# Optimization experiments

Hardware: AMD Instinct MI355X
Metric: run time of the kernel (lower is better)

The kernel has to match this reference:

```python
import jax, jax.numpy as jnp
import numpy as np

NUM_CAPSULE = 10
DIM_CAPSULE = 16
ROUTINGS = 3
EPS = 1e-7  # K.epsilon()


def squash(x, axis=-1):
    # bojone squash: x / sqrt(s2 + eps) * s2 / (1 + s2)
    s2 = jnp.sum(jnp.square(x), axis=axis, keepdims=True)
    return x * s2 / ((1.0 + s2) * jnp.sqrt(s2 + EPS))


def setup_inputs() -> dict:
    key = jax.random.key(0)
    k1, k2 = jax.random.split(key)
    B, N, D_in = 64, 2048, 128  # batch, input_num_capsule, input_dim_capsule
    u_vecs = jax.random.normal(k1, (B, N, D_in), dtype=jnp.float32)
    fan_out = NUM_CAPSULE * DIM_CAPSULE
    limit = float(np.sqrt(6.0 / (D_in + fan_out)))  # glorot_uniform
    W = jax.random.uniform(k2, (D_in, fan_out), dtype=jnp.float32,
                           minval=-limit, maxval=limit)
    return {"u_vecs": u_vecs, "W": W}


def reference(u_vecs, W):
    B, N, _ = u_vecs.shape
    # share_weights=True: conv1d with kernel size 1 == matmul over feature dim
    u_hat = (u_vecs @ W).reshape(B, N, NUM_CAPSULE, DIM_CAPSULE)
    u_hat = jnp.transpose(u_hat, (0, 2, 1, 3))  # (B, J, N, D)
    b = jnp.zeros((B, NUM_CAPSULE, N), dtype=u_vecs.dtype)
    o = jnp.zeros((B, NUM_CAPSULE, DIM_CAPSULE), dtype=u_vecs.dtype)
    for i in range(ROUTINGS):
        c = jax.nn.softmax(b, axis=1)           # softmax over output capsules
        o = jnp.einsum('bjn,bjnd->bjd', c, u_hat)
        if i < ROUTINGS - 1:
            b = jnp.einsum('bjd,bjnd->bjn', o, u_hat)  # agreement update
    return squash(o)
```

## Files before the change

### kernel.cpp

```cpp
#include <hip/hip_runtime.h>
#include <math.h>


#define BATCH 64
#define NN    2048
#define KD    128
#define JCAP  10
#define DCAP  16
#define JDIM  160
#define EPSQ  1e-7f
#define TPB   256

#define WS_SP   0
#define WS_V    65536
#define WS_GP1  147456
#define WS_O2P  802816

__global__ __launch_bounds__(TPB) void f_colsum(const float* __restrict__ u,
                                                float* __restrict__ Sp) {
  const int b = blockIdx.y, tile = blockIdx.x, t = threadIdx.x;
  const int k4 = (t & 31) * 4, rg = t >> 5;
  __shared__ float4 red[256];
  const float* p = u + ((size_t)(b * NN) + tile * 256 + rg * 32) * KD + k4;
  float4 a = make_float4(0.f, 0.f, 0.f, 0.f);
#pragma unroll 4
  for (int r = 0; r < 32; ++r) {
    float4 w = *(const float4*)(p + (size_t)r * KD);
    a.x += w.x; a.y += w.y; a.z += w.z; a.w += w.w;
  }
  red[t] = a;
  __syncthreads();
  if (t < 32) {
    float4 s4 = red[t];
#pragma unroll
    for (int rg2 = 1; rg2 < 8; ++rg2) {
      float4 w = red[rg2 * 32 + t];
      s4.x += w.x; s4.y += w.y; s4.z += w.z; s4.w += w.w;
    }
    *(float4*)&Sp[(size_t)(b * 8 + tile) * KD + t * 4] = s4;
  }
}

__global__ __launch_bounds__(TPB) void f_makeV(const float* __restrict__ ws,
                                               const float* __restrict__ W,
                                               float* __restrict__ V,
                                               int pass) {
  const int b = blockIdx.x, t = threadIdx.x;
  __shared__ float gsum[JCAP * KD];
  __shared__ float o_s[JDIM];
  if (pass == 0) {
    const float* Sp = ws + WS_SP + (size_t)b * 8 * KD;
    if (t < KD) {
      float s = 0.f;
#pragma unroll
      for (int tl = 0; tl < 8; ++tl) s += Sp[tl * KD + t];
      gsum[t] = s * 0.1f;
    }
  } else {
    const float* Gp1 = ws + WS_GP1 + (size_t)b * 8 * JCAP * KD;
    for (int i = t; i < JCAP * KD; i += TPB) {
      float s = 0.f;
#pragma unroll
      for (int tl = 0; tl < 8; ++tl) s += Gp1[tl * JCAP * KD + i];
      gsum[i] = s;
    }
  }
  __syncthreads();
  if (t < JDIM) {
    const int j = t >> 4;
    const float* gs = pass == 0 ? gsum : (gsum + j * KD);
    float acc = 0.f;
#pragma unroll 4
    for (int k = 0; k < KD; ++k) acc += gs[k] * W[k * JDIM + t];
    o_s[t] = acc;
  }
  __syncthreads();
  const int k = t & 127, gg = t >> 7;
#pragma unroll
  for (int i = 0; i < 5; ++i) {
    const int j = gg * 5 + i;
    const float* wp = W + k * JDIM + j * DCAP;
    float acc = 0.f;
#pragma unroll
    for (int d = 0; d < DCAP; ++d) acc += wp[d] * o_s[j * DCAP + d];
    V[(size_t)(b * JCAP + j) * KD + k] = acc;
  }
}

__global__ __launch_bounds__(TPB) void f_route(const float* __restrict__ u,
                                               const float* __restrict__ V,
                                               const float* __restrict__ W,
                                               float* __restrict__ dst,
                                               int pass) {
  const int b = blockIdx.y, tile = blockIdx.x, t = threadIdx.x;
  const int r0 = tile * 256;
  __shared__ __align__(16) float Cs[JCAP][260];
  __shared__ __align__(16) float Gp[4][JCAP][KD];
  {
    const float* up = u + (size_t)(b * NN + r0 + t) * KD;
    const float* vb = V + (size_t)(b * JCAP) * KD;
    float acc[JCAP];
#pragma unroll
    for (int j = 0; j < JCAP; ++j) acc[j] = 0.f;
    for (int kc = 0; kc < KD; kc += 8) {
      float4 xa = *(const float4*)(up + kc);
      float4 xb = *(const float4*)(up + kc + 4);
#pragma unroll
      for (int j = 0; j < JCAP; ++j) {
        float4 v0 = *(const float4*)(vb + j * KD + kc);
        float4 v1 = *(const float4*)(vb + j * KD + kc + 4);
        acc[j] += xa.x * v0.x + xa.y * v0.y + xa.z * v0.z + xa.w * v0.w
                + xb.x * v1.x + xb.y * v1.y + xb.z * v1.z + xb.w * v1.w;
      }
    }
    float m = acc[0];
#pragma unroll
    for (int j = 1; j < JCAP; ++j) m = fmaxf(m, acc[j]);
    float s = 0.f;
#pragma unroll
    for (int j = 0; j < JCAP; ++j) { acc[j] = __expf(acc[j] - m); s += acc[j]; }
    const float inv = 1.f / s;
#pragma unroll
    for (int j = 0; j < JCAP; ++j) Cs[j][t] = acc[j] * inv;
  }
  __syncthreads();
  {
    const int wave = t >> 6, lane = t & 63;
    const int rw = wave * 64;
    float g0[JCAP], g1[JCAP];
#pragma unroll
    for (int j = 0; j < JCAP; ++j) { g0[j] = 0.f; g1[j] = 0.f; }
    const float* ub = u + (size_t)(b * NN + r0 + rw) * KD + 2 * lane;
    for (int rc = 0; rc < 64; rc += 4) {
      float ua[4], uc[4];
#pragma unroll
      for (int q = 0; q < 4; ++q) {
        float2 w = *(const float2*)(ub + (size_t)(rc + q) * KD);
        ua[q] = w.x; uc[q] = w.y;
      }
#pragma unroll
      for (int j = 0; j < JCAP; ++j) {
        float4 c4 = *(const float4*)&Cs[j][rw + rc];
        g0[j] += c4.x * ua[0] + c4.y * ua[1] + c4.z * ua[2] + c4.w * ua[3];
        g1[j] += c4.x * uc[0] + c4.y * uc[1] + c4.z * uc[2] + c4.w * uc[3];
      }
    }
#pragma unroll
    for (int j = 0; j < JCAP; ++j)
      *(float2*)&Gp[wave][j][2 * lane] = make_float2(g0[j], g1[j]);
  }
  __syncthreads();
  if (pass == 0) {
    float* Gp1 = dst + (size_t)(b * 8 + tile) * JCAP * KD;
    for (int i = t; i < JCAP * KD; i += TPB)
      Gp1[i] = Gp[0][0][i] + Gp[1][0][i] + Gp[2][0][i] + Gp[3][0][i];
  } else {
    for (int i = t; i < JCAP * KD; i += TPB)
      Gp[0][0][i] = Gp[0][0][i] + Gp[1][0][i] + Gp[2][0][i] + Gp[3][0][i];
    __syncthreads();
    if (t < JDIM) {
      const int j = t >> 4;
      float acc = 0.f;
#pragma unroll 4
      for (int k = 0; k < KD; ++k) acc += Gp[0][j][k] * W[k * JDIM + t];
      dst[(size_t)(b * 8 + tile) * JDIM + t] = acc;
    }
  }
}

__global__ __launch_bounds__(TPB) void f_squash(const float* __restrict__ O2p,
                                                float* __restrict__ out) {
  const int b = blockIdx.x, t = threadIdx.x;
  __shared__ float o_s[JDIM];
  __shared__ float sc[JCAP];
  if (t < JDIM) {
    const float* p = O2p + (size_t)b * 8 * JDIM;
    float s = 0.f;
#pragma unroll
    for (int tl = 0; tl < 8; ++tl) s += p[tl * JDIM + t];
    o_s[t] = s;
  }
  __syncthreads();
  if (t < JCAP) {
    float s2 = 0.f;
#pragma unroll
    for (int d = 0; d < DCAP; ++d) { float x = o_s[t * DCAP + d]; s2 += x * x; }
    sc[t] = s2 / ((1.f + s2) * sqrtf(s2 + EPSQ));
  }
  __syncthreads();
  if (t < JDIM) out[b * JDIM + t] = o_s[t] * sc[t >> 4];
}

extern "C" void kernel_launch(void* const* d_in, const int* in_sizes, int n_in,
                              void* d_out, int out_size, void* d_ws, size_t ws_size,
                              hipStream_t stream) {
  const float* u = (const float*)d_in[0];
  const float* W = (const float*)d_in[1];
  float* out = (float*)d_out;
  float* ws  = (float*)d_ws;

  float* Sp  = ws + WS_SP;
  float* V   = ws + WS_V;
  float* Gp1 = ws + WS_GP1;
  float* O2p = ws + WS_O2P;
  f_colsum<<<dim3(8, BATCH), TPB, 0, stream>>>(u, Sp);
  f_makeV <<<BATCH, TPB, 0, stream>>>(ws, W, V, 0);
  f_route <<<dim3(8, BATCH), TPB, 0, stream>>>(u, V, W, Gp1, 0);
  f_makeV <<<BATCH, TPB, 0, stream>>>(ws, W, V, 1);
  f_route <<<dim3(8, BATCH), TPB, 0, stream>>>(u, V, W, O2p, 1);
  f_squash<<<BATCH, TPB, 0, stream>>>(O2p, out);
}
```

Baseline: 172.8 us.

## Fuse V construction and squash into routing kernels using last-block atomic counter

```diff
diff --git a/kernel.cpp b/kernel.cpp
--- a/kernel.cpp
+++ b/kernel.cpp
@@ -12,13 +12,16 @@
 #define TPB   256
 
 #define WS_SP   0
-#define WS_V    65536
-#define WS_GP1  147456
-#define WS_O2P  802816
-
-__global__ __launch_bounds__(TPB) void f_colsum(const float* __restrict__ u,
-                                                float* __restrict__ Sp) {
+#define WS_GP1  65536
+#define WS_O2P  720896
+#define WS_VG   802816
+#define WS_CNT  884736
+
+__global__ __launch_bounds__(TPB) void k_prep(const float* __restrict__ u,
+                                              float* __restrict__ Sp,
+                                              unsigned int* __restrict__ cnt) {
   const int b = blockIdx.y, tile = blockIdx.x, t = threadIdx.x;
+  if (b == 0 && tile == 0 && t < BATCH) cnt[t] = 0u;
   const int k4 = (t & 31) * 4, rg = t >> 5;
   __shared__ float4 red[256];
   const float* p = u + ((size_t)(b * NN) + tile * 256 + rg * 32) * KD + k4;
@@ -41,27 +44,37 @@
   }
 }
 
-__global__ __launch_bounds__(TPB) void f_makeV(const float* __restrict__ ws,
+__global__ __launch_bounds__(TPB) void k_route(const float* __restrict__ u,
+                                               const float* __restrict__ wsro,
                                                const float* __restrict__ W,
-                                               float* __restrict__ V,
+                                               float* __restrict__ Vg,
+                                               float* __restrict__ dst,
+                                               float* __restrict__ out,
+                                               unsigned int* __restrict__ cnt,
                                                int pass) {
-  const int b = blockIdx.x, t = threadIdx.x;
-  __shared__ float gsum[JCAP * KD];
+  const int b = blockIdx.y, tile = blockIdx.x, t = threadIdx.x;
+  const int r0 = tile * 256;
+  __shared__ __align__(16) float Cs[JCAP][260];
+  __shared__ __align__(16) float Gp[4][JCAP][KD];
   __shared__ float o_s[JDIM];
+  __shared__ float sc[JCAP];
+  __shared__ unsigned int lastflag;
+  float* gsum = &Gp[0][0][0];
+
   if (pass == 0) {
-    const float* Sp = ws + WS_SP + (size_t)b * 8 * KD;
+    const float* SpB = wsro + WS_SP + (size_t)b * 8 * KD;
     if (t < KD) {
       float s = 0.f;
 #pragma unroll
-      for (int tl = 0; tl < 8; ++tl) s += Sp[tl * KD + t];
+      for (int tl = 0; tl < 8; ++tl) s += SpB[tl * KD + t];
       gsum[t] = s * 0.1f;
     }
   } else {
-    const float* Gp1 = ws + WS_GP1 + (size_t)b * 8 * JCAP * KD;
+    const float* GpB = wsro + WS_GP1 + (size_t)b * 8 * (JCAP * KD);
     for (int i = t; i < JCAP * KD; i += TPB) {
       float s = 0.f;
 #pragma unroll
-      for (int tl = 0; tl < 8; ++tl) s += Gp1[tl * JCAP * KD + i];
+      for (int tl = 0; tl < 8; ++tl) s += GpB[tl * (JCAP * KD) + i];
       gsum[i] = s;
     }
   }
@@ -75,30 +88,24 @@
     o_s[t] = acc;
   }
   __syncthreads();
-  const int k = t & 127, gg = t >> 7;
-#pragma unroll
-  for (int i = 0; i < 5; ++i) {
-    const int j = gg * 5 + i;
-    const float* wp = W + k * JDIM + j * DCAP;
-    float acc = 0.f;
-#pragma unroll
-    for (int d = 0; d < DCAP; ++d) acc += wp[d] * o_s[j * DCAP + d];
-    V[(size_t)(b * JCAP + j) * KD + k] = acc;
-  }
-}
-
-__global__ __launch_bounds__(TPB) void f_route(const float* __restrict__ u,
-                                               const float* __restrict__ V,
-                                               const float* __restrict__ W,
-                                               float* __restrict__ dst,
-                                               int pass) {
-  const int b = blockIdx.y, tile = blockIdx.x, t = threadIdx.x;
-  const int r0 = tile * 256;
-  __shared__ __align__(16) float Cs[JCAP][260];
-  __shared__ __align__(16) float Gp[4][JCAP][KD];
+  {
+    const int k = t & 127, gg = t >> 7;
+    float* vb = Vg + (size_t)b * (JCAP * KD);
+#pragma unroll
+    for (int i = 0; i < 5; ++i) {
+      const int j = gg * 5 + i;
+      const float* wp = W + k * JDIM + j * DCAP;
+      float acc = 0.f;
+#pragma unroll
+      for (int d = 0; d < DCAP; ++d) acc += wp[d] * o_s[j * DCAP + d];
+      vb[j * KD + k] = acc;
+    }
+  }
+  __syncthreads();
+
   {
     const float* up = u + (size_t)(b * NN + r0 + t) * KD;
-    const float* vb = V + (size_t)(b * JCAP) * KD;
+    const float* vb = Vg + (size_t)b * (JCAP * KD);
     float acc[JCAP];
 #pragma unroll
     for (int j = 0; j < JCAP; ++j) acc[j] = 0.f;
@@ -124,6 +131,7 @@
     for (int j = 0; j < JCAP; ++j) Cs[j][t] = acc[j] * inv;
   }
   __syncthreads();
+
   {
     const int wave = t >> 6, lane = t & 63;
     const int rw = wave * 64;
@@ -145,36 +153,41 @@
         g1[j] += c4.x * uc[0] + c4.y * uc[1] + c4.z * uc[2] + c4.w * uc[3];
       }
     }
+    __syncthreads();
 #pragma unroll
     for (int j = 0; j < JCAP; ++j)
       *(float2*)&Gp[wave][j][2 * lane] = make_float2(g0[j], g1[j]);
   }
   __syncthreads();
+
   if (pass == 0) {
-    float* Gp1 = dst + (size_t)(b * 8 + tile) * JCAP * KD;
+    float* g1d = dst + (size_t)(b * 8 + tile) * (JCAP * KD);
     for (int i = t; i < JCAP * KD; i += TPB)
-      Gp1[i] = Gp[0][0][i] + Gp[1][0][i] + Gp[2][0][i] + Gp[3][0][i];
-  } else {
-    for (int i = t; i < JCAP * KD; i += TPB)
-      Gp[0][0][i] = Gp[0][0][i] + Gp[1][0][i] + Gp[2][0][i] + Gp[3][0][i];
-    __syncthreads();
-    if (t < JDIM) {
-      const int j = t >> 4;
-      float acc = 0.f;
+      g1d[i] = Gp[0][0][i] + Gp[1][0][i] + Gp[2][0][i] + Gp[3][0][i];
+    return;
+  }
+
+  for (int i = t; i < JCAP * KD; i += TPB)
+    Gp[0][0][i] = Gp[0][0][i] + Gp[1][0][i] + Gp[2][0][i] + Gp[3][0][i];
+  __syncthreads();
+  if (t < JDIM) {
+    const int j = t >> 4;
+    float acc = 0.f;
 #pragma unroll 4
-      for (int k = 0; k < KD; ++k) acc += Gp[0][j][k] * W[k * JDIM + t];
-      dst[(size_t)(b * 8 + tile) * JDIM + t] = acc;
-    }
-  }
-}
-
-__global__ __launch_bounds__(TPB) void f_squash(const float* __restrict__ O2p,
-                                                float* __restrict__ out) {
-  const int b = blockIdx.x, t = threadIdx.x;
-  __shared__ float o_s[JDIM];
-  __shared__ float sc[JCAP];
+    for (int k = 0; k < KD; ++k) acc += Gp[0][j][k] * W[k * JDIM + t];
+    dst[(size_t)(b * 8 + tile) * JDIM + t] = acc;
+  }
+  __syncthreads();
+  if (t == 0) {
+    __threadfence();
+    lastflag = atomicAdd(&cnt[b], 1u);
+  }
+  __syncthreads();
+  if (lastflag != 7u) return;
+  __threadfence();
+
+  const float* p = dst + (size_t)b * 8 * JDIM;
   if (t < JDIM) {
-    const float* p = O2p + (size_t)b * 8 * JDIM;
     float s = 0.f;
 #pragma unroll
     for (int tl = 0; tl < 8; ++tl) s += p[tl * JDIM + t];
@@ -200,13 +213,12 @@
   float* ws  = (float*)d_ws;
 
   float* Sp  = ws + WS_SP;
-  float* V   = ws + WS_V;
   float* Gp1 = ws + WS_GP1;
   float* O2p = ws + WS_O2P;
-  f_colsum<<<dim3(8, BATCH), TPB, 0, stream>>>(u, Sp);
-  f_makeV <<<BATCH, TPB, 0, stream>>>(ws, W, V, 0);
-  f_route <<<dim3(8, BATCH), TPB, 0, stream>>>(u, V, W, Gp1, 0);
-  f_makeV <<<BATCH, TPB, 0, stream>>>(ws, W, V, 1);
-  f_route <<<dim3(8, BATCH), TPB, 0, stream>>>(u, V, W, O2p, 1);
-  f_squash<<<BATCH, TPB, 0, stream>>>(O2p, out);
+  float* Vg  = ws + WS_VG;
+  unsigned int* cnt = (unsigned int*)(ws + WS_CNT);
+
+  k_prep <<<dim3(8, BATCH), TPB, 0, stream>>>(u, Sp, cnt);
+  k_route<<<dim3(8, BATCH), TPB, 0, stream>>>(u, ws, W, Vg, Gp1, out, cnt, 0);
+  k_route<<<dim3(8, BATCH), TPB, 0, stream>>>(u, ws, W, Vg, O2p, out, cnt, 1);
 }
```

After: 229.5 us. 32.8% more time.
